# Kernel tuning notes

Hardware: AMD Instinct MI355X
Metric: run time of the kernel (lower is better)

Reference implementation:

```python
import jax, jax.numpy as jnp
import numpy as np

T, D, E = 65536, 1024, 64  # tokens, d_model, n_experts

def setup_inputs() -> dict:
    key = jax.random.key(0)
    k1, k2 = jax.random.split(key)
    x = jax.random.normal(k1, (T, D), dtype=jnp.float32)
    Wg = jax.random.normal(k2, (D, E), dtype=jnp.float32) * (1.0 / np.sqrt(D))
    return {"x": x, "Wg": Wg, "top_k": 2}

def reference(x, Wg, top_k):
    # Token-to-expert gating: logits -> softmax -> top-k -> renormalized combine weights.
    logits = jnp.einsum('td,de->te', x, Wg)            # [T, E]
    probs = jax.nn.softmax(logits, axis=-1)            # [T, E]
    topk_vals, topk_idx = jax.lax.top_k(probs, top_k)  # [T, k], [T, k]
    combine = topk_vals / jnp.sum(topk_vals, axis=-1, keepdims=True)  # renormalize over selected experts
    return combine, topk_idx, probs
```

## Files before the change

kernel.cpp:

```cpp
#include <hip/hip_runtime.h>
#include <math.h>


#define D_DIM 1024
#define E_DIM 64
#define TM    128
#define KC    64
#define NCH   (D_DIM / KC)
#define TPB   256
#define MARGIN 1e-3f
#define WT_U4  16384

typedef float f32x4 __attribute__((ext_vector_type(4)));
typedef short s16x8 __attribute__((ext_vector_type(8)));

__device__ __forceinline__ unsigned bf16hi_rne(unsigned u) {
  return (u + 0x7FFFu + ((u >> 16) & 1u)) & 0xFFFF0000u;
}

__global__ void wprep_kernel(const float* __restrict__ Wg, uint4* __restrict__ w4,
                             unsigned* __restrict__ ctr) {
  const int gi = blockIdx.x * blockDim.x + threadIdx.x;
  if (gi == 0) ctr[0] = 0u;
  const int ch = gi >> 9;
  const int e  = (gi >> 3) & 63;
  const int g  = gi & 7;
  const int k0 = ch * KC + (g ^ (e & 7)) * 8;
  unsigned hp[4], lp[4];
#pragma unroll
  for (int jj = 0; jj < 4; ++jj) {
    const float w0 = Wg[(k0 + 2 * jj    ) * E_DIM + e];
    const float w1 = Wg[(k0 + 2 * jj + 1) * E_DIM + e];
    const unsigned h0 = bf16hi_rne(__float_as_uint(w0));
    const unsigned h1 = bf16hi_rne(__float_as_uint(w1));
    const float l0 = w0 - __uint_as_float(h0);
    const float l1 = w1 - __uint_as_float(h1);
    hp[jj] = h1 | (h0 >> 16);
    lp[jj] = bf16hi_rne(__float_as_uint(l1)) | (bf16hi_rne(__float_as_uint(l0)) >> 16);
  }
  w4[gi]         = make_uint4(hp[0], hp[1], hp[2], hp[3]);
  w4[8192 + gi]  = make_uint4(lp[0], lp[1], lp[2], lp[3]);
}

struct Frag2 { s16x8 hi, lo; };

__device__ __forceinline__ Frag2 cvt8(const float4 a, const float4 b) {
  const float f[8] = {a.x, a.y, a.z, a.w, b.x, b.y, b.z, b.w};
  unsigned h[8], l[8];
#pragma unroll
  for (int i = 0; i < 8; ++i) {
    const unsigned hb = bf16hi_rne(__float_as_uint(f[i]));
    const float lf = f[i] - __uint_as_float(hb);
    h[i] = hb;
    l[i] = bf16hi_rne(__float_as_uint(lf));
  }
  union { uint4 u; s16x8 v; } H, L;
  H.u = make_uint4(h[1] | (h[0] >> 16), h[3] | (h[2] >> 16),
                   h[5] | (h[4] >> 16), h[7] | (h[6] >> 16));
  L.u = make_uint4(l[1] | (l[0] >> 16), l[3] | (l[2] >> 16),
                   l[5] | (l[4] >> 16), l[7] | (l[6] >> 16));
  Frag2 r; r.hi = H.v; r.lo = L.v; return r;
}

__global__ __launch_bounds__(TPB, 2) void router_mfma(
    const float* __restrict__ x, const uint4* __restrict__ wt,
    float* __restrict__ out, unsigned* __restrict__ ctr,
    unsigned* __restrict__ list, int rcap, int T)
{
  __shared__ uint4 sw[2][1024];

  const int tid   = threadIdx.x;
  const int wid   = tid >> 6;
  const int lane  = tid & 63;
  const int c     = lane & 15;
  const int q     = lane >> 4;
  const int twave = blockIdx.x * TM + wid * 32;

  f32x4 acc[4][2];
#pragma unroll
  for (int et = 0; et < 4; ++et)
#pragma unroll
    for (int tt = 0; tt < 2; ++tt)
      acc[et][tt] = (f32x4){0.f, 0.f, 0.f, 0.f};

  const float* xb0 = x + (size_t)(twave + c) * D_DIM + q * 8;
  const float* xb1 = xb0 + (size_t)16 * D_DIM;

  uint4  wr[4];
  float4 xr[8];

#pragma unroll
  for (int i = 0; i < 4; ++i) wr[i] = wt[(i >> 1) * 8192 + (i & 1) * 256 + tid];
#pragma unroll
  for (int i = 0; i < 4; ++i) sw[0][(i >> 1) * 512 + (i & 1) * 256 + tid] = wr[i];
#pragma unroll
  for (int v = 0; v < 8; ++v) {
    const int tt = v >> 2, s = (v >> 1) & 1, h = v & 1;
    const float* b = (tt ? xb1 : xb0);
    xr[v] = *(const float4*)(b + s * 32 + h * 4);
  }
#pragma unroll
  for (int i = 0; i < 4; ++i) wr[i] = wt[(i >> 1) * 8192 + 512 + (i & 1) * 256 + tid];
  __syncthreads();

  const int row0 = c * 64;
  const int g0 = ((0 + q) ^ (c & 7)) * 8;
  const int g1 = ((4 + q) ^ (c & 7)) * 8;

  for (int ch = 0; ch < NCH; ++ch) {
    const int cur = ch & 1;
    if (ch + 1 < NCH) {
#pragma unroll
      for (int i = 0; i < 4; ++i)
        sw[cur ^ 1][(i >> 1) * 512 + (i & 1) * 256 + tid] = wr[i];
    }
    if (ch + 2 < NCH) {
#pragma unroll
      for (int i = 0; i < 4; ++i)
        wr[i] = wt[(i >> 1) * 8192 + (ch + 2) * 512 + (i & 1) * 256 + tid];
    }

    Frag2 bx[2][2];
#pragma unroll
    for (int tt = 0; tt < 2; ++tt)
#pragma unroll
      for (int s = 0; s < 2; ++s)
        bx[tt][s] = cvt8(xr[tt * 4 + s * 2 + 0], xr[tt * 4 + s * 2 + 1]);

    if (ch + 1 < NCH) {
#pragma unroll
      for (int v = 0; v < 8; ++v) {
        const int tt = v >> 2, s = (v >> 1) & 1, h = v & 1;
        const float* b = (tt ? xb1 : xb0);
        xr[v] = *(const float4*)(b + (ch + 1) * KC + s * 32 + h * 4);
      }
    }

    const ushort* bufh = (const ushort*)&sw[cur][0];
    const ushort* bufl = bufh + 4096;
#pragma unroll
    for (int s = 0; s < 2; ++s) {
      const int go = s ? g1 : g0;
      s16x8 ah[4], al[4];
#pragma unroll
      for (int et = 0; et < 4; ++et) {
        ah[et] = *(const s16x8*)(bufh + et * 1024 + row0 + go);
        al[et] = *(const s16x8*)(bufl + et * 1024 + row0 + go);
      }
#pragma unroll
      for (int et = 0; et < 4; ++et)
#pragma unroll
        for (int tt = 0; tt < 2; ++tt) {
          f32x4 a = acc[et][tt];
          a = __builtin_amdgcn_mfma_f32_16x16x32_bf16(ah[et], bx[tt][s].hi, a, 0, 0, 0);
          a = __builtin_amdgcn_mfma_f32_16x16x32_bf16(ah[et], bx[tt][s].lo, a, 0, 0, 0);
          a = __builtin_amdgcn_mfma_f32_16x16x32_bf16(al[et], bx[tt][s].hi, a, 0, 0, 0);
          acc[et][tt] = a;
        }
    }
    __syncthreads();
  }

  const size_t Ts = (size_t)T;
  float* const comb = out;
  float* const idxo = out + 2 * Ts;
  float* const prob = out + 4 * Ts;

#pragma unroll
  for (int tt = 0; tt < 2; ++tt) {
    const int tok = twave + tt * 16 + c;
    float v[16];
#pragma unroll
    for (int et = 0; et < 4; ++et)
#pragma unroll
      for (int r = 0; r < 4; ++r) v[et * 4 + r] = acc[et][tt][r];

    float v1 = v[0], v2 = -INFINITY, v3 = -INFINITY;
    int   i1 = q * 4, i2 = 0;
#pragma unroll
    for (int et = 0; et < 4; ++et)
#pragma unroll
      for (int r = 0; r < 4; ++r) {
        if (et == 0 && r == 0) continue;
        const float p  = v[et * 4 + r];
        const int   ei = et * 16 + q * 4 + r;
        if (p > v1)      { v3 = v2; v2 = v1; i2 = i1; v1 = p; i1 = ei; }
        else if (p > v2) { v3 = v2; v2 = p;  i2 = ei; }
        else if (p > v3) { v3 = p; }
      }
#pragma unroll
    for (int d = 16; d <= 32; d <<= 1) {
      const float ov1 = __shfl_xor(v1, d); const int oi1 = __shfl_xor(i1, d);
      const float ov2 = __shfl_xor(v2, d); const int oi2 = __shfl_xor(i2, d);
      const float ov3 = __shfl_xor(v3, d);
      const bool  ob1 = (ov1 > v1) || (ov1 == v1 && oi1 < i1);
      const float w1v = ob1 ? ov1 : v1;  const int w1i = ob1 ? oi1 : i1;
      const float l1v = ob1 ? v1  : ov1; const int l1i = ob1 ? i1  : oi1;
      const float w2v = ob1 ? ov2 : v2;  const int w2i = ob1 ? oi2 : i2;
      const float ls2 = ob1 ? v2  : ov2;
      const float ws3 = ob1 ? ov3 : v3;
      const bool  b2  = (l1v > w2v) || (l1v == w2v && l1i < w2i);
      const float a2v = b2 ? l1v : w2v; const int a2i = b2 ? l1i : w2i;
      const float a3v = b2 ? fmaxf(w2v, ls2) : fmaxf(l1v, ws3);
      v1 = w1v; i1 = w1i; v2 = a2v; i2 = a2i; v3 = a3v;
    }

    float s = 0.f;
#pragma unroll
    for (int i = 0; i < 16; ++i) { v[i] = __expf(v[i] - v1); s += v[i]; }
    s += __shfl_xor(s, 16);
    s += __shfl_xor(s, 32);
    const float inv = 1.f / s;

#pragma unroll
    for (int et = 0; et < 4; ++et)
      *(float4*)&prob[(size_t)tok * E_DIM + et * 16 + q * 4] =
          make_float4(v[et * 4 + 0] * inv, v[et * 4 + 1] * inv,
                      v[et * 4 + 2] * inv, v[et * 4 + 3] * inv);

    if (q == 0) {
      if ((v1 - v2 < MARGIN) || (v2 - v3 < MARGIN)) {
        const unsigned slot = atomicAdd(ctr, 1u);
        if ((int)slot < rcap) list[slot] = (unsigned)tok;
      }
      const float c1 = 1.f / (1.f + __expf(v2 - v1));
      *(float2*)&comb[2 * (size_t)tok] = make_float2(c1, 1.f - c1);
      *(float2*)&idxo[2 * (size_t)tok] = make_float2((float)i1, (float)i2);
    }
  }
}

__global__ __launch_bounds__(256) void repair_kernel(
    const float* __restrict__ x, const float* __restrict__ Wg,
    float* __restrict__ out, const unsigned* __restrict__ ctr,
    const unsigned* __restrict__ list, int rcap, int T)
{
  __shared__ double part[4][E_DIM];
  const int tid = threadIdx.x;
  const int e   = tid & 63;
  const int s   = tid >> 6;
  const unsigned total = ctr[0];
  const unsigned n = total < (unsigned)rcap ? total : (unsigned)rcap;

  for (unsigned j = blockIdx.x; j < n; j += gridDim.x) {
    const int t = (int)list[j];
    const float* xr = x  + (size_t)t * D_DIM + s * 256;
    const float* wr = Wg + (size_t)(s * 256) * E_DIM + e;
    double a = 0.0;
#pragma unroll 8
    for (int d = 0; d < 256; ++d)
      a += (double)xr[d] * (double)wr[(size_t)d * E_DIM];
    part[s][e] = a;
    __syncthreads();
    if (tid < 64) {
      const float l = (float)(part[0][e] + part[1][e] + part[2][e] + part[3][e]);
      float m = l;
#pragma unroll
      for (int d2 = 1; d2 < 64; d2 <<= 1) m = fmaxf(m, __shfl_xor(m, d2));
      const float p = expf(l - m);
      float ss = p;
#pragma unroll
      for (int d2 = 1; d2 < 64; d2 <<= 1) ss += __shfl_xor(ss, d2);
      out[4 * (size_t)T + (size_t)t * E_DIM + e] = p / ss;
      float v1 = l, v2 = -INFINITY; int i1 = e, i2 = 0;
#pragma unroll
      for (int d2 = 1; d2 < 64; d2 <<= 1) {
        const float ov1 = __shfl_xor(v1, d2); const int oi1 = __shfl_xor(i1, d2);
        const float ov2 = __shfl_xor(v2, d2); const int oi2 = __shfl_xor(i2, d2);
        const bool  ob1 = (ov1 > v1) || (ov1 == v1 && oi1 < i1);
        const float w1v = ob1 ? ov1 : v1;  const int w1i = ob1 ? oi1 : i1;
        const float l1v = ob1 ? v1  : ov1; const int l1i = ob1 ? i1  : oi1;
        const float w2v = ob1 ? ov2 : v2;  const int w2i = ob1 ? oi2 : i2;
        const bool  b2  = (l1v > w2v) || (l1v == w2v && l1i < w2i);
        v1 = w1v; i1 = w1i;
        v2 = b2 ? l1v : w2v; i2 = b2 ? l1i : w2i;
      }
      if (e == 0) {
        const float c1 = 1.f / (1.f + expf(v2 - v1));
        out[2 * (size_t)t]     = c1;
        out[2 * (size_t)t + 1] = 1.f - c1;
        out[2 * (size_t)T + 2 * (size_t)t]     = (float)i1;
        out[2 * (size_t)T + 2 * (size_t)t + 1] = (float)i2;
      }
    }
    __syncthreads();
  }
}

extern "C" void kernel_launch(void* const* d_in, const int* in_sizes, int n_in,
                              void* d_out, int out_size, void* d_ws, size_t ws_size,
                              hipStream_t stream) {
  const float* x  = (const float*)d_in[0];
  const float* Wg = (const float*)d_in[1];
  float* out = (float*)d_out;
  uint4* wt  = (uint4*)d_ws;
  unsigned* ctr  = (unsigned*)d_ws + WT_U4 * 4;
  unsigned* list = ctr + 1;
  const int T = in_sizes[0] / D_DIM;

  long avail = ((long)ws_size - (long)(WT_U4 * 16 + 4)) / 4;
  int rcap = avail < 0 ? 0 : (avail > 8192 ? 8192 : (int)avail);

  wprep_kernel<<<dim3(NCH * E_DIM * 8 / TPB), dim3(TPB), 0, stream>>>(Wg, wt, ctr);
  router_mfma<<<dim3(T / TM), dim3(TPB), 0, stream>>>(x, wt, out, ctr, list, rcap, T);
  repair_kernel<<<dim3(1024), dim3(256), 0, stream>>>(x, Wg, out, ctr, list, rcap, T);
}
```

Measured before the change: 420.4 us.

## Read gate weights directly from global memory, drop LDS staging, halve tokens per block

The router kernel no longer stages the bf16 hi/lo weight chunks through double-buffered shared memory with barriers. Each lane now loads its MFMA A-fragments straight from global memory, relying on cache, since every block reads the same 256 KB. Each wave now handles 16 tokens instead of 32, the block tile drops to 64 tokens, and launch bounds ask for 4 blocks per CU. x loads are double-buffered across two register sets, and the bf16 conversion now uses the HIP intrinsic. This removes LDS traffic and syncs, at the cost of more redundant global/L2 weight reads per token and less weight reuse per wave.

Result: slower. 474.8 us (+12.9%).

```diff
diff --git a/kernel.cpp b/kernel.cpp
--- a/kernel.cpp
+++ b/kernel.cpp
@@ -1,10 +1,11 @@
 #include <hip/hip_runtime.h>
+#include <hip/hip_bf16.h>
 #include <math.h>
 
 
 #define D_DIM 1024
 #define E_DIM 64
-#define TM    128
+#define TM    64
 #define KC    64
 #define NCH   (D_DIM / KC)
 #define TPB   256
@@ -14,8 +15,10 @@
 typedef float f32x4 __attribute__((ext_vector_type(4)));
 typedef short s16x8 __attribute__((ext_vector_type(8)));
 
-__device__ __forceinline__ unsigned bf16hi_rne(unsigned u) {
-  return (u + 0x7FFFu + ((u >> 16) & 1u)) & 0xFFFF0000u;
+__device__ __forceinline__ ushort bf16u(float f) {
+  union { __hip_bfloat16 b; ushort u; } cv;
+  cv.b = __float2bfloat16(f);
+  return cv.u;
 }
 
 __global__ void wprep_kernel(const float* __restrict__ Wg, uint4* __restrict__ w4,
@@ -25,140 +28,108 @@
   const int ch = gi >> 9;
   const int e  = (gi >> 3) & 63;
   const int g  = gi & 7;
-  const int k0 = ch * KC + (g ^ (e & 7)) * 8;
+  const int k0 = ch * KC + g * 8;
   unsigned hp[4], lp[4];
 #pragma unroll
   for (int jj = 0; jj < 4; ++jj) {
     const float w0 = Wg[(k0 + 2 * jj    ) * E_DIM + e];
     const float w1 = Wg[(k0 + 2 * jj + 1) * E_DIM + e];
-    const unsigned h0 = bf16hi_rne(__float_as_uint(w0));
-    const unsigned h1 = bf16hi_rne(__float_as_uint(w1));
+    const unsigned h0 = (unsigned)bf16u(w0) << 16;
+    const unsigned h1 = (unsigned)bf16u(w1) << 16;
     const float l0 = w0 - __uint_as_float(h0);
     const float l1 = w1 - __uint_as_float(h1);
-    hp[jj] = h1 | (h0 >> 16);
-    lp[jj] = bf16hi_rne(__float_as_uint(l1)) | (bf16hi_rne(__float_as_uint(l0)) >> 16);
-  }
-  w4[gi]         = make_uint4(hp[0], hp[1], hp[2], hp[3]);
-  w4[8192 + gi]  = make_uint4(lp[0], lp[1], lp[2], lp[3]);
+    hp[jj] = (h1) | (h0 >> 16);
+    lp[jj] = ((unsigned)bf16u(l1) << 16) | (unsigned)bf16u(l0);
+  }
+  w4[gi]        = make_uint4(hp[0], hp[1], hp[2], hp[3]);
+  w4[8192 + gi] = make_uint4(lp[0], lp[1], lp[2], lp[3]);
 }
 
 struct Frag2 { s16x8 hi, lo; };
 
 __device__ __forceinline__ Frag2 cvt8(const float4 a, const float4 b) {
   const float f[8] = {a.x, a.y, a.z, a.w, b.x, b.y, b.z, b.w};
-  unsigned h[8], l[8];
+  Frag2 r;
 #pragma unroll
   for (int i = 0; i < 8; ++i) {
-    const unsigned hb = bf16hi_rne(__float_as_uint(f[i]));
-    const float lf = f[i] - __uint_as_float(hb);
-    h[i] = hb;
-    l[i] = bf16hi_rne(__float_as_uint(lf));
-  }
-  union { uint4 u; s16x8 v; } H, L;
-  H.u = make_uint4(h[1] | (h[0] >> 16), h[3] | (h[2] >> 16),
-                   h[5] | (h[4] >> 16), h[7] | (h[6] >> 16));
-  L.u = make_uint4(l[1] | (l[0] >> 16), l[3] | (l[2] >> 16),
-                   l[5] | (l[4] >> 16), l[7] | (l[6] >> 16));
-  Frag2 r; r.hi = H.v; r.lo = L.v; return r;
-}
-
-__global__ __launch_bounds__(TPB, 2) void router_mfma(
+    const ushort h = bf16u(f[i]);
+    r.hi[i] = (short)h;
+    const float lf = f[i] - __uint_as_float((unsigned)h << 16);
+    r.lo[i] = (short)bf16u(lf);
+  }
+  return r;
+}
+
+__global__ __launch_bounds__(TPB, 4) void router_mfma(
     const float* __restrict__ x, const uint4* __restrict__ wt,
     float* __restrict__ out, unsigned* __restrict__ ctr,
     unsigned* __restrict__ list, int rcap, int T)
 {
-  __shared__ uint4 sw[2][1024];
-
   const int tid   = threadIdx.x;
   const int wid   = tid >> 6;
   const int lane  = tid & 63;
   const int c     = lane & 15;
   const int q     = lane >> 4;
-  const int twave = blockIdx.x * TM + wid * 32;
-
-  f32x4 acc[4][2];
-#pragma unroll
-  for (int et = 0; et < 4; ++et)
-#pragma unroll
-    for (int tt = 0; tt < 2; ++tt)
-      acc[et][tt] = (f32x4){0.f, 0.f, 0.f, 0.f};
-
-  const float* xb0 = x + (size_t)(twave + c) * D_DIM + q * 8;
-  const float* xb1 = xb0 + (size_t)16 * D_DIM;
-
-  uint4  wr[4];
-  float4 xr[8];
-
-#pragma unroll
-  for (int i = 0; i < 4; ++i) wr[i] = wt[(i >> 1) * 8192 + (i & 1) * 256 + tid];
-#pragma unroll
-  for (int i = 0; i < 4; ++i) sw[0][(i >> 1) * 512 + (i & 1) * 256 + tid] = wr[i];
-#pragma unroll
-  for (int v = 0; v < 8; ++v) {
-    const int tt = v >> 2, s = (v >> 1) & 1, h = v & 1;
-    const float* b = (tt ? xb1 : xb0);
-    xr[v] = *(const float4*)(b + s * 32 + h * 4);
-  }
-#pragma unroll
-  for (int i = 0; i < 4; ++i) wr[i] = wt[(i >> 1) * 8192 + 512 + (i & 1) * 256 + tid];
-  __syncthreads();
-
-  const int row0 = c * 64;
-  const int g0 = ((0 + q) ^ (c & 7)) * 8;
-  const int g1 = ((4 + q) ^ (c & 7)) * 8;
-
-  for (int ch = 0; ch < NCH; ++ch) {
-    const int cur = ch & 1;
-    if (ch + 1 < NCH) {
-#pragma unroll
-      for (int i = 0; i < 4; ++i)
-        sw[cur ^ 1][(i >> 1) * 512 + (i & 1) * 256 + tid] = wr[i];
+  const int tok   = blockIdx.x * TM + wid * 16 + c;
+
+  f32x4 acc[4];
+#pragma unroll
+  for (int et = 0; et < 4; ++et) acc[et] = (f32x4){0.f, 0.f, 0.f, 0.f};
+
+  const float* __restrict__ xb = x + (size_t)tok * D_DIM + q * 8;
+  const uint4* __restrict__ wl = wt + c * 8 + q;
+
+  float4 xA[4], xB[4];
+#pragma unroll
+  for (int v = 0; v < 4; ++v) {
+    const int s = v >> 1, h = v & 1;
+    xA[v] = *(const float4*)(xb + s * 32 + h * 4);
+    xB[v] = *(const float4*)(xb + KC + s * 32 + h * 4);
+  }
+
+  auto step = [&](float4 (&xr)[4], int ch) {
+    s16x8 a0h[4], a0l[4];
+#pragma unroll
+    for (int et = 0; et < 4; ++et) {
+      a0h[et] = *(const s16x8*)(wl + (size_t)ch * 512 + et * 128);
+      a0l[et] = *(const s16x8*)(wl + (size_t)ch * 512 + 8192 + et * 128);
+    }
+    const Frag2 b0 = cvt8(xr[0], xr[1]);
+    const Frag2 b1 = cvt8(xr[2], xr[3]);
+#pragma unroll
+    for (int et = 0; et < 4; ++et) {
+      f32x4 a = acc[et];
+      a = __builtin_amdgcn_mfma_f32_16x16x32_bf16(a0h[et], b0.hi, a, 0, 0, 0);
+      a = __builtin_amdgcn_mfma_f32_16x16x32_bf16(a0h[et], b0.lo, a, 0, 0, 0);
+      a = __builtin_amdgcn_mfma_f32_16x16x32_bf16(a0l[et], b0.hi, a, 0, 0, 0);
+      acc[et] = a;
     }
     if (ch + 2 < NCH) {
 #pragma unroll
-      for (int i = 0; i < 4; ++i)
-        wr[i] = wt[(i >> 1) * 8192 + (ch + 2) * 512 + (i & 1) * 256 + tid];
-    }
-
-    Frag2 bx[2][2];
-#pragma unroll
-    for (int tt = 0; tt < 2; ++tt)
-#pragma unroll
-      for (int s = 0; s < 2; ++s)
-        bx[tt][s] = cvt8(xr[tt * 4 + s * 2 + 0], xr[tt * 4 + s * 2 + 1]);
-
-    if (ch + 1 < NCH) {
-#pragma unroll
-      for (int v = 0; v < 8; ++v) {
-        const int tt = v >> 2, s = (v >> 1) & 1, h = v & 1;
-        const float* b = (tt ? xb1 : xb0);
-        xr[v] = *(const float4*)(b + (ch + 1) * KC + s * 32 + h * 4);
+      for (int v = 0; v < 4; ++v) {
+        const int s = v >> 1, h = v & 1;
+        xr[v] = *(const float4*)(xb + (ch + 2) * KC + s * 32 + h * 4);
       }
     }
-
-    const ushort* bufh = (const ushort*)&sw[cur][0];
-    const ushort* bufl = bufh + 4096;
-#pragma unroll
-    for (int s = 0; s < 2; ++s) {
-      const int go = s ? g1 : g0;
-      s16x8 ah[4], al[4];
-#pragma unroll
-      for (int et = 0; et < 4; ++et) {
-        ah[et] = *(const s16x8*)(bufh + et * 1024 + row0 + go);
-        al[et] = *(const s16x8*)(bufl + et * 1024 + row0 + go);
-      }
-#pragma unroll
-      for (int et = 0; et < 4; ++et)
-#pragma unroll
-        for (int tt = 0; tt < 2; ++tt) {
-          f32x4 a = acc[et][tt];
-          a = __builtin_amdgcn_mfma_f32_16x16x32_bf16(ah[et], bx[tt][s].hi, a, 0, 0, 0);
-          a = __builtin_amdgcn_mfma_f32_16x16x32_bf16(ah[et], bx[tt][s].lo, a, 0, 0, 0);
-          a = __builtin_amdgcn_mfma_f32_16x16x32_bf16(al[et], bx[tt][s].hi, a, 0, 0, 0);
-          acc[et][tt] = a;
-        }
-    }
-    __syncthreads();
+    s16x8 a1h[4], a1l[4];
+#pragma unroll
+    for (int et = 0; et < 4; ++et) {
+      a1h[et] = *(const s16x8*)(wl + (size_t)ch * 512 + et * 128 + 4);
+      a1l[et] = *(const s16x8*)(wl + (size_t)ch * 512 + 8192 + et * 128 + 4);
+    }
+#pragma unroll
+    for (int et = 0; et < 4; ++et) {
+      f32x4 a = acc[et];
+      a = __builtin_amdgcn_mfma_f32_16x16x32_bf16(a1h[et], b1.hi, a, 0, 0, 0);
+      a = __builtin_amdgcn_mfma_f32_16x16x32_bf16(a1h[et], b1.lo, a, 0, 0, 0);
+      a = __builtin_amdgcn_mfma_f32_16x16x32_bf16(a1l[et], b1.hi, a, 0, 0, 0);
+      acc[et] = a;
+    }
+  };
+
+  for (int ch = 0; ch < NCH; ch += 2) {
+    step(xA, ch);
+    step(xB, ch + 1);
   }
 
   const size_t Ts = (size_t)T;
@@ -166,67 +137,63 @@
   float* const idxo = out + 2 * Ts;
   float* const prob = out + 4 * Ts;
 
-#pragma unroll
-  for (int tt = 0; tt < 2; ++tt) {
-    const int tok = twave + tt * 16 + c;
-    float v[16];
-#pragma unroll
-    for (int et = 0; et < 4; ++et)
-#pragma unroll
-      for (int r = 0; r < 4; ++r) v[et * 4 + r] = acc[et][tt][r];
-
-    float v1 = v[0], v2 = -INFINITY, v3 = -INFINITY;
-    int   i1 = q * 4, i2 = 0;
-#pragma unroll
-    for (int et = 0; et < 4; ++et)
-#pragma unroll
-      for (int r = 0; r < 4; ++r) {
-        if (et == 0 && r == 0) continue;
-        const float p  = v[et * 4 + r];
-        const int   ei = et * 16 + q * 4 + r;
-        if (p > v1)      { v3 = v2; v2 = v1; i2 = i1; v1 = p; i1 = ei; }
-        else if (p > v2) { v3 = v2; v2 = p;  i2 = ei; }
-        else if (p > v3) { v3 = p; }
-      }
-#pragma unroll
-    for (int d = 16; d <= 32; d <<= 1) {
-      const float ov1 = __shfl_xor(v1, d); const int oi1 = __shfl_xor(i1, d);
-      const float ov2 = __shfl_xor(v2, d); const int oi2 = __shfl_xor(i2, d);
-      const float ov3 = __shfl_xor(v3, d);
-      const bool  ob1 = (ov1 > v1) || (ov1 == v1 && oi1 < i1);
-      const float w1v = ob1 ? ov1 : v1;  const int w1i = ob1 ? oi1 : i1;
-      const float l1v = ob1 ? v1  : ov1; const int l1i = ob1 ? i1  : oi1;
-      const float w2v = ob1 ? ov2 : v2;  const int w2i = ob1 ? oi2 : i2;
-      const float ls2 = ob1 ? v2  : ov2;
-      const float ws3 = ob1 ? ov3 : v3;
-      const bool  b2  = (l1v > w2v) || (l1v == w2v && l1i < w2i);
-      const float a2v = b2 ? l1v : w2v; const int a2i = b2 ? l1i : w2i;
-      const float a3v = b2 ? fmaxf(w2v, ls2) : fmaxf(l1v, ws3);
-      v1 = w1v; i1 = w1i; v2 = a2v; i2 = a2i; v3 = a3v;
-    }
-
-    float s = 0.f;
-#pragma unroll
-    for (int i = 0; i < 16; ++i) { v[i] = __expf(v[i] - v1); s += v[i]; }
-    s += __shfl_xor(s, 16);
-    s += __shfl_xor(s, 32);
-    const float inv = 1.f / s;
-
-#pragma unroll
-    for (int et = 0; et < 4; ++et)
-      *(float4*)&prob[(size_t)tok * E_DIM + et * 16 + q * 4] =
-          make_float4(v[et * 4 + 0] * inv, v[et * 4 + 1] * inv,
-                      v[et * 4 + 2] * inv, v[et * 4 + 3] * inv);
-
-    if (q == 0) {
-      if ((v1 - v2 < MARGIN) || (v2 - v3 < MARGIN)) {
-        const unsigned slot = atomicAdd(ctr, 1u);
-        if ((int)slot < rcap) list[slot] = (unsigned)tok;
-      }
-      const float c1 = 1.f / (1.f + __expf(v2 - v1));
-      *(float2*)&comb[2 * (size_t)tok] = make_float2(c1, 1.f - c1);
-      *(float2*)&idxo[2 * (size_t)tok] = make_float2((float)i1, (float)i2);
-    }
+  float v[16];
+#pragma unroll
+  for (int et = 0; et < 4; ++et)
+#pragma unroll
+    for (int r = 0; r < 4; ++r) v[et * 4 + r] = acc[et][r];
+
+  float v1 = v[0], v2 = -INFINITY, v3 = -INFINITY;
+  int   i1 = q * 4, i2 = 0;
+#pragma unroll
+  for (int et = 0; et < 4; ++et)
+#pragma unroll
+    for (int r = 0; r < 4; ++r) {
+      if (et == 0 && r == 0) continue;
+      const float p  = v[et * 4 + r];
+      const int   ei = et * 16 + q * 4 + r;
+      if (p > v1)      { v3 = v2; v2 = v1; i2 = i1; v1 = p; i1 = ei; }
+      else if (p > v2) { v3 = v2; v2 = p;  i2 = ei; }
+      else if (p > v3) { v3 = p; }
+    }
+#pragma unroll
+  for (int d = 16; d <= 32; d <<= 1) {
+    const float ov1 = __shfl_xor(v1, d); const int oi1 = __shfl_xor(i1, d);
+    const float ov2 = __shfl_xor(v2, d); const int oi2 = __shfl_xor(i2, d);
+    const float ov3 = __shfl_xor(v3, d);
+    const bool  ob1 = (ov1 > v1) || (ov1 == v1 && oi1 < i1);
+    const float w1v = ob1 ? ov1 : v1;  const int w1i = ob1 ? oi1 : i1;
+    const float l1v = ob1 ? v1  : ov1; const int l1i = ob1 ? i1  : oi1;
+    const float w2v = ob1 ? ov2 : v2;  const int w2i = ob1 ? oi2 : i2;
+    const float ls2 = ob1 ? v2  : ov2;
+    const float ws3 = ob1 ? ov3 : v3;
+    const bool  b2  = (l1v > w2v) || (l1v == w2v && l1i < w2i);
+    const float a2v = b2 ? l1v : w2v; const int a2i = b2 ? l1i : w2i;
+    const float a3v = b2 ? fmaxf(w2v, ls2) : fmaxf(l1v, ws3);
+    v1 = w1v; i1 = w1i; v2 = a2v; i2 = a2i; v3 = a3v;
+  }
+
+  float s = 0.f;
+#pragma unroll
+  for (int i = 0; i < 16; ++i) { v[i] = __expf(v[i] - v1); s += v[i]; }
+  s += __shfl_xor(s, 16);
+  s += __shfl_xor(s, 32);
+  const float inv = 1.f / s;
+
+#pragma unroll
+  for (int et = 0; et < 4; ++et)
+    *(float4*)&prob[(size_t)tok * E_DIM + et * 16 + q * 4] =
+        make_float4(v[et * 4 + 0] * inv, v[et * 4 + 1] * inv,
+                    v[et * 4 + 2] * inv, v[et * 4 + 3] * inv);
+
+  if (q == 0) {
+    if ((v1 - v2 < MARGIN) || (v2 - v3 < MARGIN)) {
+      const unsigned slot = atomicAdd(ctr, 1u);
+      if ((int)slot < rcap) list[slot] = (unsigned)tok;
+    }
+    const float c1 = 1.f / (1.f + __expf(v2 - v1));
+    *(float2*)&comb[2 * (size_t)tok] = make_float2(c1, 1.f - c1);
+    *(float2*)&idxo[2 * (size_t)tok] = make_float2((float)i1, (float)i2);
   }
 }
 
```
